# Optimization experiments

Measured on AMD Instinct MI355X. Metric: run time of the kernel, lower is better.

## Reference

```python
import jax, jax.numpy as jnp
import numpy as np

B_FACTOR = 4          # branching factor of the complete tree
DEPTH = 7             # levels 0..DEPTH; level DEPTH are leaves
N_NODES = (B_FACTOR ** (DEPTH + 1) - 1) // (B_FACTOR - 1)   # 21845
N_INTERNAL = (B_FACTOR ** DEPTH - 1) // (B_FACTOR - 1)      # 5461
IN_SIZE = 512
HID = 512
PARAM_SCALE = 0.02


def setup_inputs() -> dict:
    key = jax.random.key(0)
    ks = jax.random.split(key, 7)
    x = jax.random.normal(ks[0], (N_NODES, IN_SIZE), dtype=jnp.float32)
    # torch nn.Linear parameters: y = x @ W.T + b
    W_iou = jax.random.normal(ks[1], (3 * HID, IN_SIZE), dtype=jnp.float32) * PARAM_SCALE
    b_iou = jax.random.normal(ks[2], (3 * HID,), dtype=jnp.float32) * PARAM_SCALE
    W_f = jax.random.normal(ks[3], (HID, IN_SIZE), dtype=jnp.float32) * PARAM_SCALE
    b_f = jax.random.normal(ks[4], (HID,), dtype=jnp.float32) * PARAM_SCALE
    U_iou = jax.random.normal(ks[5], (3 * HID, HID), dtype=jnp.float32) * PARAM_SCALE
    U_f = jax.random.normal(ks[6], (HID, HID), dtype=jnp.float32) * PARAM_SCALE
    # children[j] = indices of the 4 children of internal node j (complete 4-ary tree)
    children = (B_FACTOR * jnp.arange(N_INTERNAL, dtype=jnp.int32)[:, None]
                + jnp.arange(1, B_FACTOR + 1, dtype=jnp.int32)[None, :])
    return {"x": x, "children": children, "W_iou": W_iou, "b_iou": b_iou,
            "W_f": W_f, "b_f": b_f, "U_iou": U_iou, "U_f": U_f}


def reference(x, children, W_iou, b_iou, W_f, b_f, U_iou, U_f):
    """Child-Sum Tree-LSTM over a complete 4-ary tree, processed level-batched
    bottom-up (equivalent to the per-node postorder recursion in the source).
    Leaves keep h = c = 0, as in the source (_forward_postorder returns early).
    NOTE: the source applies NO sigmoid to the forget gate term; we keep that.
    """
    N = x.shape[0]
    H = U_f.shape[0]
    # input-dependent parts are tree-independent: precompute once for all nodes
    wx_iou = x @ W_iou.T + b_iou          # [N, 3H]
    wx_f = x @ W_f.T + b_f                # [N, H]
    h = jnp.zeros((N, H), dtype=x.dtype)
    c = jnp.zeros_like(h)
    # level l occupies node indices [offs[l], offs[l+1]) — static constants
    offs = [(B_FACTOR ** l - 1) // (B_FACTOR - 1) for l in range(DEPTH + 2)]
    for l in range(DEPTH - 1, -1, -1):    # internal levels, deepest first
        s, e = offs[l], offs[l + 1]
        ch = children[s:e]                # [M, 4]
        h_ch = h[ch]                      # [M, 4, H] gather of child hidden states
        c_ch = c[ch]                      # [M, 4, H]
        h_sum = h_ch.sum(axis=1)          # child-sum
        iou = wx_iou[s:e] + h_sum @ U_iou.T               # [M, 3H]
        i, o, u = jnp.split(iou, 3, axis=-1)
        i = jax.nn.sigmoid(i)
        o = jax.nn.sigmoid(o)
        u = jnp.tanh(u)
        # forget term per child (no sigmoid, faithful to source)
        f = wx_f[s:e][:, None, :] + h_ch @ U_f.T          # [M, 4, H]
        c_new = i * u + (f * c_ch).sum(axis=1)            # [M, H]
        h = h.at[s:e].set(o * jnp.tanh(c_new))
        c = c.at[s:e].set(c_new)
    return h, c
```

## Files before the change

### kernel.cpp

```cpp
#include <hip/hip_runtime.h>
#include <cmath>

constexpr int N_NODES = 21845;
constexpr int N_INT   = 5461;
constexpr int HID     = 512;

typedef short  short8  __attribute__((ext_vector_type(8)));
typedef float  floatx4 __attribute__((ext_vector_type(4)));

__device__ __forceinline__ unsigned short f2bf(float f) {
    unsigned int u = __float_as_uint(f);
    u += 0x7fffu + ((u >> 16) & 1u);
    return (unsigned short)(u >> 16);
}

__global__ void prep_kernel(const float* __restrict__ x,
                            const float* __restrict__ W_iou,
                            const float* __restrict__ W_f,
                            const float* __restrict__ U_iou,
                            const float* __restrict__ U_f,
                            float* __restrict__ h_leaf,
                            float* __restrict__ c_leaf,
                            unsigned short* __restrict__ dstb)
{
    const size_t Z  = (size_t)(N_NODES - N_INT) * HID / 4;
    const size_t C0 = (size_t)N_INT * 512 / 4;
    const size_t C1 = C0 + 1536 * 512 / 4;
    const size_t C2 = C1 + 512 * 512 / 4;
    const size_t C3 = C2 + 1536 * 512 / 4;
    const size_t C4 = C3 + 512 * 512 / 4;
    const size_t total = 2 * Z + C4;
    size_t i = (size_t)blockIdx.x * blockDim.x + threadIdx.x;
    const size_t stride = (size_t)gridDim.x * blockDim.x;
    const float4 zz = {0.f, 0.f, 0.f, 0.f};
    for (; i < total; i += stride) {
        if (i < 2 * Z) {
            if (i < Z) ((float4*)h_leaf)[i] = zz;
            else       ((float4*)c_leaf)[i - Z] = zz;
        } else {
            size_t k = i - 2 * Z;
            const float* src; size_t off;
            if (k < C0)      { src = x;     off = k; }
            else if (k < C1) { src = W_iou; off = k - C0; }
            else if (k < C2) { src = W_f;   off = k - C1; }
            else if (k < C3) { src = U_iou; off = k - C2; }
            else             { src = U_f;   off = k - C3; }
            float4 v = ((const float4*)src)[off];
            ushort4 o;
            o.x = f2bf(v.x); o.y = f2bf(v.y); o.z = f2bf(v.z); o.w = f2bf(v.w);
            ((ushort4*)dstb)[k] = o;
        }
    }
}

#define GLD_LDS(g, l) __builtin_amdgcn_global_load_lds( \
    (const __attribute__((address_space(1))) void*)(g), \
    (__attribute__((address_space(3))) void*)(l), 16, 0, 0)

__device__ __forceinline__ void gemm_tile_128(
    const unsigned short* __restrict__ A, int Arows,
    const unsigned short* __restrict__ B,
    const float* __restrict__ bias,
    float* __restrict__ C, int ldc,
    int bm, int bn)
{
    __shared__ short8 AsV[1024];
    __shared__ short8 BsV[1024];

    const int tid  = threadIdx.x;
    const int wave = tid >> 6;
    const int lane = tid & 63;
    const int quad = lane >> 4;
    const int lr   = lane & 15;
    const int wr = (wave >> 1) * 64;
    const int wc = (wave & 1) * 64;

    floatx4 acc[4][4];
    #pragma unroll
    for (int i = 0; i < 4; ++i)
        #pragma unroll
        for (int j = 0; j < 4; ++j)
            acc[i][j] = (floatx4){0.f, 0.f, 0.f, 0.f};

    int s_row[4], s_gk[4];
    #pragma unroll
    for (int it = 0; it < 4; ++it) {
        int c = it * 256 + wave * 64 + lane;
        s_row[it] = c >> 3;
        s_gk[it]  = (c & 7) ^ (s_row[it] & 7);
    }

    for (int k0 = 0; k0 < 512; k0 += 64) {
        #pragma unroll
        for (int it = 0; it < 4; ++it) {
            int row = s_row[it];
            int gm = bm + row; if (gm >= Arows) gm = Arows - 1;
            GLD_LDS(A + (size_t)gm * 512 + k0 + s_gk[it] * 8, &AsV[it * 256 + wave * 64]);
            int gn = bn + row;
            GLD_LDS(B + (size_t)gn * 512 + k0 + s_gk[it] * 8, &BsV[it * 256 + wave * 64]);
        }
        __syncthreads();

        #pragma unroll
        for (int kc = 0; kc < 2; ++kc) {
            short8 af[4], bfr[4];
            const int q = kc * 4 + quad;
            #pragma unroll
            for (int mt = 0; mt < 4; ++mt) {
                int row = wr + mt * 16 + lr;
                af[mt] = AsV[row * 8 + (q ^ (row & 7))];
            }
            #pragma unroll
            for (int nt = 0; nt < 4; ++nt) {
                int row = wc + nt * 16 + lr;
                bfr[nt] = BsV[row * 8 + (q ^ (row & 7))];
            }
            #pragma unroll
            for (int mt = 0; mt < 4; ++mt)
                #pragma unroll
                for (int nt = 0; nt < 4; ++nt)
                    acc[mt][nt] = __builtin_amdgcn_mfma_f32_16x16x32_bf16(
                        af[mt], bfr[nt], acc[mt][nt], 0, 0, 0);
        }
        __syncthreads();
    }

    #pragma unroll
    for (int mt = 0; mt < 4; ++mt) {
        #pragma unroll
        for (int r = 0; r < 4; ++r) {
            int gm = bm + wr + mt * 16 + quad * 4 + r;
            if (gm >= Arows) continue;
            #pragma unroll
            for (int nt = 0; nt < 4; ++nt) {
                int gn = bn + wc + nt * 16 + lr;
                float v = acc[mt][nt][r];
                if (bias) v += bias[gn];
                C[(size_t)gm * ldc + gn] = v;
            }
        }
    }
}

__global__ __launch_bounds__(256) void wgemm_kernel(
    const unsigned short* __restrict__ xb,
    const unsigned short* __restrict__ Wib,
    const unsigned short* __restrict__ Wfb,
    const float* __restrict__ b_iou, const float* __restrict__ b_f,
    float* __restrict__ wx_iou, float* __restrict__ wx_f)
{
    int b = blockIdx.x;
    if (b < 516) {
        gemm_tile_128(xb, N_INT, Wib, b_iou, wx_iou, 1536, (b / 12) * 128, (b % 12) * 128);
    } else {
        int b2 = b - 516;
        gemm_tile_128(xb, 1365, Wfb, b_f, wx_f, 512, (b2 / 4) * 128, (b2 % 4) * 128);
    }
}

__global__ __launch_bounds__(256) void gemm5_kernel(
    const unsigned short* __restrict__ hs_bf,
    const unsigned short* __restrict__ h6_bf,
    const unsigned short* __restrict__ Uib, const unsigned short* __restrict__ Ufb,
    float* __restrict__ ioud, float* __restrict__ fd)
{
    int b = blockIdx.x;
    if (b < 96) {
        gemm_tile_128(hs_bf, 1024, Uib, nullptr, ioud, 1536, (b / 12) * 128, (b % 12) * 128);
    } else {
        int b2 = b - 96;
        gemm_tile_128(h6_bf, 4096, Ufb, nullptr, fd, 512, (b2 / 4) * 128, (b2 % 4) * 128);
    }
}

__global__ __launch_bounds__(256) void gemm4_kernel(
    const unsigned short* __restrict__ hs_bf,
    const unsigned short* __restrict__ h5_bf,
    const unsigned short* __restrict__ Uib, const unsigned short* __restrict__ Ufb,
    float* __restrict__ ioud, float* __restrict__ fd)
{
    int b = blockIdx.x;
    if (b < 24) {
        gemm_tile_128(hs_bf, 256, Uib, nullptr, ioud, 1536, (b / 12) * 128, (b % 12) * 128);
    } else {
        int b2 = b - 24;
        gemm_tile_128(h5_bf, 1024, Ufb, nullptr, fd, 512, (b2 / 4) * 128, (b2 % 4) * 128);
    }
}

__device__ __forceinline__ void direct_tile_16x64(
    const unsigned short* __restrict__ A, int Arows,
    const unsigned short* __restrict__ B,
    float* __restrict__ C, int ldc,
    int m0, int n0)
{
    const int lane = threadIdx.x & 63;
    const int quad = lane >> 4;
    const int lr   = lane & 15;
    int am = m0 + lr; if (am >= Arows) am = Arows - 1;
    const unsigned short* ap = A + (size_t)am * 512 + quad * 8;
    const unsigned short* bp = B + (size_t)(n0 + lr) * 512 + quad * 8;

    floatx4 acc[4];
    #pragma unroll
    for (int j = 0; j < 4; ++j) acc[j] = (floatx4){0.f, 0.f, 0.f, 0.f};

    #pragma unroll
    for (int k0 = 0; k0 < 512; k0 += 32) {
        short8 af = *(const short8*)(ap + k0);
        #pragma unroll
        for (int j = 0; j < 4; ++j) {
            short8 bf = *(const short8*)(bp + (size_t)j * 16 * 512 + k0);
            acc[j] = __builtin_amdgcn_mfma_f32_16x16x32_bf16(af, bf, acc[j], 0, 0, 0);
        }
    }

    #pragma unroll
    for (int j = 0; j < 4; ++j) {
        #pragma unroll
        for (int r = 0; r < 4; ++r) {
            int gm = m0 + quad * 4 + r;
            if (gm < Arows) C[(size_t)gm * ldc + n0 + j * 16 + lr] = acc[j][r];
        }
    }
}

__global__ __launch_bounds__(256) void gemm_small_kernel(
    const unsigned short* __restrict__ hs_bf,
    const unsigned short* __restrict__ hch_bf,
    const unsigned short* __restrict__ Uib, const unsigned short* __restrict__ Ufb,
    float* __restrict__ ioud, float* __restrict__ fd, int nl)
{
    const int w = blockIdx.x * 4 + (threadIdx.x >> 6);
    const int mI = (nl + 15) >> 4;
    const int nI = 1536 / 64;
    const int mF = (4 * nl + 15) >> 4;
    if (w < mI * nI) {
        direct_tile_16x64(hs_bf, nl, Uib, ioud, 1536, (w / nI) * 16, (w % nI) * 64);
    } else {
        int w2 = w - mI * nI;
        if (w2 < mF * 8)
            direct_tile_16x64(hch_bf, 4 * nl, Ufb, fd, 512, (w2 / 8) * 16, (w2 % 8) * 64);
    }
}

__global__ __launch_bounds__(512) void combine_wide_kernel(
    const float* __restrict__ wx_iou, const float* __restrict__ wx_f,
    const float* __restrict__ ioud, const float* __restrict__ fd,
    const float* __restrict__ c_child,
    float* __restrict__ h_out, float* __restrict__ c_out,
    unsigned short* __restrict__ h_bf, unsigned short* __restrict__ hs_bf,
    int s, int np)
{
    __shared__ float4 hsbuf[512];
    const int k  = threadIdx.x >> 7;
    const int jg = threadIdx.x & 127;
    const int j4 = jg << 2;
    const bool hasU = (ioud != nullptr);

    for (int tp = blockIdx.x; tp < np; tp += gridDim.x) {
        const int t = 4 * tp + k;
        const int n = s + t;
        const float* wrow = wx_iou + (size_t)n * 1536 + j4;
        float4 iv = *(const float4*)(wrow);
        float4 ov = *(const float4*)(wrow + 512);
        float4 uv = *(const float4*)(wrow + 1024);
        float4 fc = {0.f, 0.f, 0.f, 0.f};
        if (hasU) {
            const float* drow = ioud + (size_t)t * 1536 + j4;
            float4 a  = *(const float4*)(drow);
            float4 b  = *(const float4*)(drow + 512);
            float4 u2 = *(const float4*)(drow + 1024);
            float4 wf = *(const float4*)(wx_f + (size_t)n * 512 + j4);
            #pragma unroll
            for (int c = 0; c < 4; ++c) {
                ((float*)&iv)[c] += ((float*)&a)[c];
                ((float*)&ov)[c] += ((float*)&b)[c];
                ((float*)&uv)[c] += ((float*)&u2)[c];
            }
            #pragma unroll
            for (int q = 0; q < 4; ++q) {
                float4 f  = *(const float4*)(fd + (size_t)(4 * t + q) * 512 + j4);
                float4 cv = *(const float4*)(c_child + (size_t)(4 * t + q) * 512 + j4);
                #pragma unroll
                for (int c = 0; c < 4; ++c)
                    ((float*)&fc)[c] += (((float*)&wf)[c] + ((float*)&f)[c]) * ((float*)&cv)[c];
            }
        }
        float4 cn, hn; ushort4 hb;
        #pragma unroll
        for (int c = 0; c < 4; ++c) {
            float ig = 1.f / (1.f + expf(-((float*)&iv)[c]));
            float og = 1.f / (1.f + expf(-((float*)&ov)[c]));
            float ug = tanhf(((float*)&uv)[c]);
            float cv2 = ig * ug + ((float*)&fc)[c];
            float hv = og * tanhf(cv2);
            ((float*)&cn)[c] = cv2;
            ((float*)&hn)[c] = hv;
            ((unsigned short*)&hb)[c] = f2bf(hv);
        }
        *(float4*)(c_out + (size_t)n * 512 + j4) = cn;
        *(float4*)(h_out + (size_t)n * 512 + j4) = hn;
        *(ushort4*)(h_bf + (size_t)n * 512 + j4) = hb;
        hsbuf[threadIdx.x] = hn;
        __syncthreads();
        if (threadIdx.x < 128) {
            float4 s0 = hsbuf[jg], s1 = hsbuf[128 + jg], s2 = hsbuf[256 + jg], s3 = hsbuf[384 + jg];
            ushort4 ho;
            #pragma unroll
            for (int c = 0; c < 4; ++c)
                ((unsigned short*)&ho)[c] =
                    f2bf(((float*)&s0)[c] + ((float*)&s1)[c] + ((float*)&s2)[c] + ((float*)&s3)[c]);
            *(ushort4*)(hs_bf + (size_t)tp * 512 + j4) = ho;
        }
        __syncthreads();
    }
}

__global__ __launch_bounds__(128) void combine_root_kernel(
    const float* __restrict__ wx_iou, const float* __restrict__ wx_f,
    const float* __restrict__ ioud, const float* __restrict__ fd,
    const float* __restrict__ c_child,
    float* __restrict__ h_out, float* __restrict__ c_out)
{
    const int j4 = threadIdx.x << 2;
    float4 iv = *(const float4*)(wx_iou + j4);
    float4 ov = *(const float4*)(wx_iou + 512 + j4);
    float4 uv = *(const float4*)(wx_iou + 1024 + j4);
    float4 a  = *(const float4*)(ioud + j4);
    float4 b  = *(const float4*)(ioud + 512 + j4);
    float4 u2 = *(const float4*)(ioud + 1024 + j4);
    float4 wf = *(const float4*)(wx_f + j4);
    float4 fc = {0.f, 0.f, 0.f, 0.f};
    #pragma unroll
    for (int c = 0; c < 4; ++c) {
        ((float*)&iv)[c] += ((float*)&a)[c];
        ((float*)&ov)[c] += ((float*)&b)[c];
        ((float*)&uv)[c] += ((float*)&u2)[c];
    }
    #pragma unroll
    for (int q = 0; q < 4; ++q) {
        float4 f  = *(const float4*)(fd + (size_t)q * 512 + j4);
        float4 cv = *(const float4*)(c_child + (size_t)q * 512 + j4);
        #pragma unroll
        for (int c = 0; c < 4; ++c)
            ((float*)&fc)[c] += (((float*)&wf)[c] + ((float*)&f)[c]) * ((float*)&cv)[c];
    }
    float4 cn, hn;
    #pragma unroll
    for (int c = 0; c < 4; ++c) {
        float ig = 1.f / (1.f + expf(-((float*)&iv)[c]));
        float og = 1.f / (1.f + expf(-((float*)&ov)[c]));
        float ug = tanhf(((float*)&uv)[c]);
        float cv2 = ig * ug + ((float*)&fc)[c];
        ((float*)&cn)[c] = cv2;
        ((float*)&hn)[c] = og * tanhf(cv2);
    }
    *(float4*)(c_out + j4) = cn;
    *(float4*)(h_out + j4) = hn;
}

extern "C" void kernel_launch(void* const* d_in, const int* in_sizes, int n_in,
                              void* d_out, int out_size, void* d_ws, size_t ws_size,
                              hipStream_t stream) {
    const float* x     = (const float*)d_in[0];
    const float* W_iou = (const float*)d_in[2];
    const float* b_iou = (const float*)d_in[3];
    const float* W_f   = (const float*)d_in[4];
    const float* b_f   = (const float*)d_in[5];
    const float* U_iou = (const float*)d_in[6];
    const float* U_f   = (const float*)d_in[7];

    float* h_out = (float*)d_out;
    float* c_out = h_out + (size_t)N_NODES * HID;

    float* ws     = (float*)d_ws;
    float* wx_iou = ws;
    float* wx_f   = wx_iou + (size_t)N_INT * 1536;
    float* ioud   = wx_f   + (size_t)1365 * 512;
    float* fd     = ioud   + (size_t)1024 * 1536;
    unsigned short* xb   = (unsigned short*)(fd + (size_t)4096 * 512);
    unsigned short* Wib  = xb  + (size_t)N_INT * 512;
    unsigned short* Wfb  = Wib + (size_t)1536 * 512;
    unsigned short* Uib  = Wfb + (size_t)512 * 512;
    unsigned short* Ufb  = Uib + (size_t)1536 * 512;
    unsigned short* h_bf = Ufb + (size_t)512 * 512;
    unsigned short* hs_bf= h_bf + (size_t)N_INT * 512;

    const int offs[9] = {0, 1, 5, 21, 85, 341, 1365, 5461, 21845};

    prep_kernel<<<2048, 256, 0, stream>>>(x, W_iou, W_f, U_iou, U_f,
                                          h_out + (size_t)N_INT * HID,
                                          c_out + (size_t)N_INT * HID, xb);

    wgemm_kernel<<<516 + 44, 256, 0, stream>>>(xb, Wib, Wfb, b_iou, b_f, wx_iou, wx_f);

    combine_wide_kernel<<<1024, 512, 0, stream>>>(
        wx_iou, nullptr, nullptr, nullptr, nullptr,
        h_out, c_out, h_bf, hs_bf, 1365, 1024);

    gemm5_kernel<<<224, 256, 0, stream>>>(hs_bf, h_bf + (size_t)1365 * HID, Uib, Ufb, ioud, fd);
    combine_wide_kernel<<<256, 512, 0, stream>>>(
        wx_iou, wx_f, ioud, fd, c_out + (size_t)1365 * HID,
        h_out, c_out, h_bf, hs_bf, 341, 256);

    gemm4_kernel<<<56, 256, 0, stream>>>(hs_bf, h_bf + (size_t)341 * HID, Uib, Ufb, ioud, fd);
    combine_wide_kernel<<<64, 512, 0, stream>>>(
        wx_iou, wx_f, ioud, fd, c_out + (size_t)341 * HID,
        h_out, c_out, h_bf, hs_bf, 85, 64);

    for (int l = 3; l >= 1; --l) {
        const int s  = offs[l];
        const int nl = offs[l + 1] - s;
        const int cb = offs[l + 1];
        const int mI = (nl + 15) >> 4;
        const int mF = (4 * nl + 15) >> 4;
        const int waves = mI * 24 + mF * 8;
        gemm_small_kernel<<<(waves + 3) / 4, 256, 0, stream>>>(
            hs_bf, h_bf + (size_t)cb * HID, Uib, Ufb, ioud, fd, nl);
        combine_wide_kernel<<<(nl + 3) / 4, 512, 0, stream>>>(
            wx_iou, wx_f, ioud, fd, c_out + (size_t)cb * HID,
            h_out, c_out, h_bf, hs_bf, s, nl >> 2);
    }

    gemm_small_kernel<<<8, 256, 0, stream>>>(
        hs_bf, h_bf + (size_t)1 * HID, Uib, Ufb, ioud, fd, 1);
    combine_root_kernel<<<1, 128, 0, stream>>>(
        wx_iou, wx_f, ioud, fd, c_out + (size_t)1 * HID, h_out, c_out);
}
```

Baseline: 275.5 us.

## Fuse all tree levels into one persistent cooperative kernel with grid syncs

Replaces the sequence of about fifteen small kernel launches (prep, input GEMM, per-level recurrent GEMMs and combines, root) with one cooperative persistent kernel. Phases are separated by grid.sync, and grid-stride loops spread each phase's tiles over a grid sized from occupancy, capped at three blocks per CU. The goal is to remove launch gaps and tail idle time on the small upper levels. The cost is that the large input GEMM and prep now run under a capped grid with launch_bounds(256,2) register limits, and each grid-wide barrier carries its own overhead. A fallback multi-kernel path is kept, and the combine step is rewritten for 256 threads handling 8 columns each.

```diff
diff --git a/kernel.cpp b/kernel.cpp
--- a/kernel.cpp
+++ b/kernel.cpp
@@ -1,5 +1,8 @@
 #include <hip/hip_runtime.h>
+#include <hip/hip_cooperative_groups.h>
 #include <cmath>
+
+namespace cg = cooperative_groups;
 
 constexpr int N_NODES = 21845;
 constexpr int N_INT   = 5461;
@@ -14,14 +17,18 @@
     return (unsigned short)(u >> 16);
 }
 
-__global__ void prep_kernel(const float* __restrict__ x,
-                            const float* __restrict__ W_iou,
-                            const float* __restrict__ W_f,
-                            const float* __restrict__ U_iou,
-                            const float* __restrict__ U_f,
-                            float* __restrict__ h_leaf,
-                            float* __restrict__ c_leaf,
-                            unsigned short* __restrict__ dstb)
+#define GLD_LDS(g, l) __builtin_amdgcn_global_load_lds( \
+    (const __attribute__((address_space(1))) void*)(g), \
+    (__attribute__((address_space(3))) void*)(l), 16, 0, 0)
+
+__device__ __forceinline__ void prep_body(const float* __restrict__ x,
+                                          const float* __restrict__ W_iou,
+                                          const float* __restrict__ W_f,
+                                          const float* __restrict__ U_iou,
+                                          const float* __restrict__ U_f,
+                                          float* __restrict__ h_leaf,
+                                          float* __restrict__ c_leaf,
+                                          unsigned short* __restrict__ dstb)
 {
     const size_t Z  = (size_t)(N_NODES - N_INT) * HID / 4;
     const size_t C0 = (size_t)N_INT * 512 / 4;
@@ -53,10 +60,6 @@
     }
 }
 
-#define GLD_LDS(g, l) __builtin_amdgcn_global_load_lds( \
-    (const __attribute__((address_space(1))) void*)(g), \
-    (__attribute__((address_space(3))) void*)(l), 16, 0, 0)
-
 __device__ __forceinline__ void gemm_tile_128(
     const unsigned short* __restrict__ A, int Arows,
     const unsigned short* __restrict__ B,
@@ -142,6 +145,268 @@
     }
 }
 
+__device__ __forceinline__ void direct_tile_16x64(
+    const unsigned short* __restrict__ A, int Arows,
+    const unsigned short* __restrict__ B,
+    float* __restrict__ C, int ldc,
+    int m0, int n0)
+{
+    const int lane = threadIdx.x & 63;
+    const int quad = lane >> 4;
+    const int lr   = lane & 15;
+    int am = m0 + lr; if (am >= Arows) am = Arows - 1;
+    const unsigned short* ap = A + (size_t)am * 512 + quad * 8;
+    const unsigned short* bp = B + (size_t)(n0 + lr) * 512 + quad * 8;
+
+    floatx4 acc[4];
+    #pragma unroll
+    for (int j = 0; j < 4; ++j) acc[j] = (floatx4){0.f, 0.f, 0.f, 0.f};
+
+    #pragma unroll
+    for (int k0 = 0; k0 < 512; k0 += 32) {
+        short8 af = *(const short8*)(ap + k0);
+        #pragma unroll
+        for (int j = 0; j < 4; ++j) {
+            short8 bf = *(const short8*)(bp + (size_t)j * 16 * 512 + k0);
+            acc[j] = __builtin_amdgcn_mfma_f32_16x16x32_bf16(af, bf, acc[j], 0, 0, 0);
+        }
+    }
+
+    #pragma unroll
+    for (int j = 0; j < 4; ++j) {
+        #pragma unroll
+        for (int r = 0; r < 4; ++r) {
+            int gm = m0 + quad * 4 + r;
+            if (gm < Arows) C[(size_t)gm * ldc + n0 + j * 16 + lr] = acc[j][r];
+        }
+    }
+}
+
+__device__ __forceinline__ void small_gemm_phase(
+    const unsigned short* __restrict__ hs_bf,
+    const unsigned short* __restrict__ hch_bf,
+    const unsigned short* __restrict__ Uib, const unsigned short* __restrict__ Ufb,
+    float* __restrict__ ioud, float* __restrict__ fd, int nl)
+{
+    const int mI = (nl + 15) >> 4;
+    const int mF = (4 * nl + 15) >> 4;
+    const int totW = mI * 24 + mF * 8;
+    for (int w = blockIdx.x * 4 + (threadIdx.x >> 6); w < totW; w += gridDim.x * 4) {
+        if (w < mI * 24)
+            direct_tile_16x64(hs_bf, nl, Uib, ioud, 1536, (w / 24) * 16, (w % 24) * 64);
+        else {
+            int w2 = w - mI * 24;
+            direct_tile_16x64(hch_bf, 4 * nl, Ufb, fd, 512, (w2 / 8) * 16, (w2 % 8) * 64);
+        }
+    }
+}
+
+__device__ void combine_level_256(
+    const float* __restrict__ wx_iou, const float* __restrict__ wx_f,
+    const float* __restrict__ ioud, const float* __restrict__ fd,
+    const float* __restrict__ c_child,
+    float* __restrict__ h_out, float* __restrict__ c_out,
+    unsigned short* __restrict__ h_bf, unsigned short* __restrict__ hs_bf,
+    int s, int np, int hasU)
+{
+    __shared__ floatx4 hsbuf[512];
+    const int k  = threadIdx.x >> 6;
+    const int jg = threadIdx.x & 63;
+    const int j8 = jg << 3;
+
+    for (int tp = blockIdx.x; tp < np; tp += gridDim.x) {
+        const int t = 4 * tp + k;
+        const int n = s + t;
+        const float* wrow = wx_iou + (size_t)n * 1536 + j8;
+        floatx4 iv0 = *(const floatx4*)(wrow);
+        floatx4 iv1 = *(const floatx4*)(wrow + 4);
+        floatx4 ov0 = *(const floatx4*)(wrow + 512);
+        floatx4 ov1 = *(const floatx4*)(wrow + 516);
+        floatx4 uv0 = *(const floatx4*)(wrow + 1024);
+        floatx4 uv1 = *(const floatx4*)(wrow + 1028);
+        floatx4 fc0 = (floatx4){0.f,0.f,0.f,0.f};
+        floatx4 fc1 = (floatx4){0.f,0.f,0.f,0.f};
+        if (hasU) {
+            const float* drow = ioud + (size_t)t * 1536 + j8;
+            iv0 += *(const floatx4*)(drow);        iv1 += *(const floatx4*)(drow + 4);
+            ov0 += *(const floatx4*)(drow + 512);  ov1 += *(const floatx4*)(drow + 516);
+            uv0 += *(const floatx4*)(drow + 1024); uv1 += *(const floatx4*)(drow + 1028);
+            const float* wfp = wx_f + (size_t)n * 512 + j8;
+            floatx4 wf0 = *(const floatx4*)(wfp);
+            floatx4 wf1 = *(const floatx4*)(wfp + 4);
+            #pragma unroll
+            for (int q = 0; q < 4; ++q) {
+                const float* fp = fd + (size_t)(4 * t + q) * 512 + j8;
+                const float* cp = c_child + (size_t)(4 * t + q) * 512 + j8;
+                floatx4 f0 = *(const floatx4*)(fp),  f1 = *(const floatx4*)(fp + 4);
+                floatx4 cv0 = *(const floatx4*)(cp), cv1 = *(const floatx4*)(cp + 4);
+                fc0 += (wf0 + f0) * cv0;
+                fc1 += (wf1 + f1) * cv1;
+            }
+        }
+        floatx4 cn0, cn1, hn0, hn1;
+        #pragma unroll
+        for (int c = 0; c < 4; ++c) {
+            float ig = 1.f / (1.f + expf(-iv0[c]));
+            float og = 1.f / (1.f + expf(-ov0[c]));
+            float ug = tanhf(uv0[c]);
+            float cv2 = ig * ug + fc0[c];
+            cn0[c] = cv2;
+            hn0[c] = og * tanhf(cv2);
+        }
+        #pragma unroll
+        for (int c = 0; c < 4; ++c) {
+            float ig = 1.f / (1.f + expf(-iv1[c]));
+            float og = 1.f / (1.f + expf(-ov1[c]));
+            float ug = tanhf(uv1[c]);
+            float cv2 = ig * ug + fc1[c];
+            cn1[c] = cv2;
+            hn1[c] = og * tanhf(cv2);
+        }
+        float* cop = c_out + (size_t)n * 512 + j8;
+        float* hop = h_out + (size_t)n * 512 + j8;
+        *(floatx4*)(cop)     = cn0;  *(floatx4*)(cop + 4) = cn1;
+        *(floatx4*)(hop)     = hn0;  *(floatx4*)(hop + 4) = hn1;
+        ushort4 hb0, hb1;
+        hb0.x = f2bf(hn0[0]); hb0.y = f2bf(hn0[1]); hb0.z = f2bf(hn0[2]); hb0.w = f2bf(hn0[3]);
+        hb1.x = f2bf(hn1[0]); hb1.y = f2bf(hn1[1]); hb1.z = f2bf(hn1[2]); hb1.w = f2bf(hn1[3]);
+        *(ushort4*)(h_bf + (size_t)n * 512 + j8)     = hb0;
+        *(ushort4*)(h_bf + (size_t)n * 512 + j8 + 4) = hb1;
+
+        hsbuf[k * 128 + jg * 2]     = hn0;
+        hsbuf[k * 128 + jg * 2 + 1] = hn1;
+        __syncthreads();
+        if (threadIdx.x < 64) {
+            const int g = threadIdx.x;
+            floatx4 s0 = hsbuf[g*2]   + hsbuf[128 + g*2]   + hsbuf[256 + g*2]   + hsbuf[384 + g*2];
+            floatx4 s1 = hsbuf[g*2+1] + hsbuf[128 + g*2+1] + hsbuf[256 + g*2+1] + hsbuf[384 + g*2+1];
+            ushort4 o0, o1;
+            o0.x = f2bf(s0[0]); o0.y = f2bf(s0[1]); o0.z = f2bf(s0[2]); o0.w = f2bf(s0[3]);
+            o1.x = f2bf(s1[0]); o1.y = f2bf(s1[1]); o1.z = f2bf(s1[2]); o1.w = f2bf(s1[3]);
+            *(ushort4*)(hs_bf + (size_t)tp * 512 + g * 8)     = o0;
+            *(ushort4*)(hs_bf + (size_t)tp * 512 + g * 8 + 4) = o1;
+        }
+        __syncthreads();
+    }
+}
+
+__global__ __launch_bounds__(256, 2) void mega_kernel(
+    const float* __restrict__ x,
+    const float* __restrict__ W_iou, const float* __restrict__ b_iou,
+    const float* __restrict__ W_f,   const float* __restrict__ b_f,
+    const float* __restrict__ U_iou, const float* __restrict__ U_f,
+    float* __restrict__ h_out, float* __restrict__ c_out,
+    float* __restrict__ wx_iou, float* __restrict__ wx_f,
+    float* __restrict__ ioud, float* __restrict__ fd,
+    unsigned short* __restrict__ xb,
+    unsigned short* __restrict__ Wib, unsigned short* __restrict__ Wfb,
+    unsigned short* __restrict__ Uib, unsigned short* __restrict__ Ufb,
+    unsigned short* __restrict__ h_bf, unsigned short* __restrict__ hs_bf)
+{
+    cg::grid_group grid = cg::this_grid();
+
+    prep_body(x, W_iou, W_f, U_iou, U_f,
+              h_out + (size_t)N_INT * HID, c_out + (size_t)N_INT * HID, xb);
+    grid.sync();
+
+    for (int b = blockIdx.x; b < 560; b += gridDim.x) {
+        if (b < 516)
+            gemm_tile_128(xb, N_INT, Wib, b_iou, wx_iou, 1536, (b / 12) * 128, (b % 12) * 128);
+        else {
+            int b2 = b - 516;
+            gemm_tile_128(xb, 1365, Wfb, b_f, wx_f, 512, (b2 / 4) * 128, (b2 % 4) * 128);
+        }
+    }
+    grid.sync();
+
+    combine_level_256(wx_iou, nullptr, nullptr, nullptr, nullptr,
+                      h_out, c_out, h_bf, hs_bf, 1365, 1024, 0);
+    grid.sync();
+
+    for (int b = blockIdx.x; b < 224; b += gridDim.x) {
+        if (b < 96)
+            gemm_tile_128(hs_bf, 1024, Uib, nullptr, ioud, 1536, (b / 12) * 128, (b % 12) * 128);
+        else {
+            int b2 = b - 96;
+            gemm_tile_128(h_bf + (size_t)1365 * HID, 4096, Ufb, nullptr, fd, 512,
+                          (b2 / 4) * 128, (b2 % 4) * 128);
+        }
+    }
+    grid.sync();
+
+    combine_level_256(wx_iou, wx_f, ioud, fd, c_out + (size_t)1365 * HID,
+                      h_out, c_out, h_bf, hs_bf, 341, 256, 1);
+    grid.sync();
+
+    for (int b = blockIdx.x; b < 56; b += gridDim.x) {
+        if (b < 24)
+            gemm_tile_128(hs_bf, 256, Uib, nullptr, ioud, 1536, (b / 12) * 128, (b % 12) * 128);
+        else {
+            int b2 = b - 24;
+            gemm_tile_128(h_bf + (size_t)341 * HID, 1024, Ufb, nullptr, fd, 512,
+                          (b2 / 4) * 128, (b2 % 4) * 128);
+        }
+    }
+    grid.sync();
+
+    combine_level_256(wx_iou, wx_f, ioud, fd, c_out + (size_t)341 * HID,
+                      h_out, c_out, h_bf, hs_bf, 85, 64, 1);
+    grid.sync();
+
+    small_gemm_phase(hs_bf, h_bf + (size_t)85 * HID, Uib, Ufb, ioud, fd, 64);
+    grid.sync();
+    combine_level_256(wx_iou, wx_f, ioud, fd, c_out + (size_t)85 * HID,
+                      h_out, c_out, h_bf, hs_bf, 21, 16, 1);
+    grid.sync();
+    small_gemm_phase(hs_bf, h_bf + (size_t)21 * HID, Uib, Ufb, ioud, fd, 16);
+    grid.sync();
+    combine_level_256(wx_iou, wx_f, ioud, fd, c_out + (size_t)21 * HID,
+                      h_out, c_out, h_bf, hs_bf, 5, 4, 1);
+    grid.sync();
+    small_gemm_phase(hs_bf, h_bf + (size_t)5 * HID, Uib, Ufb, ioud, fd, 4);
+    grid.sync();
+    combine_level_256(wx_iou, wx_f, ioud, fd, c_out + (size_t)5 * HID,
+                      h_out, c_out, h_bf, hs_bf, 1, 1, 1);
+    grid.sync();
+
+    small_gemm_phase(hs_bf, h_bf + (size_t)1 * HID, Uib, Ufb, ioud, fd, 1);
+    grid.sync();
+
+    if (blockIdx.x == 0) {
+        const int j = threadIdx.x * 2;
+        #pragma unroll
+        for (int c = 0; c < 2; ++c) {
+            const int jj = j + c;
+            float iv = wx_iou[jj]        + ioud[jj];
+            float ov = wx_iou[512 + jj]  + ioud[512 + jj];
+            float uv = wx_iou[1024 + jj] + ioud[1024 + jj];
+            float wf = wx_f[jj];
+            float fc = 0.f;
+            #pragma unroll
+            for (int q = 0; q < 4; ++q)
+                fc += (wf + fd[(size_t)q * 512 + jj]) * c_out[(size_t)(q + 1) * 512 + jj];
+            float ig = 1.f / (1.f + expf(-iv));
+            float og = 1.f / (1.f + expf(-ov));
+            float ug = tanhf(uv);
+            float cv2 = ig * ug + fc;
+            c_out[jj] = cv2;
+            h_out[jj] = og * tanhf(cv2);
+        }
+    }
+}
+
+__global__ void prep_kernel(const float* __restrict__ x,
+                            const float* __restrict__ W_iou,
+                            const float* __restrict__ W_f,
+                            const float* __restrict__ U_iou,
+                            const float* __restrict__ U_f,
+                            float* __restrict__ h_leaf,
+                            float* __restrict__ c_leaf,
+                            unsigned short* __restrict__ dstb)
+{
+    prep_body(x, W_iou, W_f, U_iou, U_f, h_leaf, c_leaf, dstb);
+}
+
 __global__ __launch_bounds__(256) void wgemm_kernel(
     const unsigned short* __restrict__ xb,
     const unsigned short* __restrict__ Wib,
@@ -188,43 +453,6 @@
     }
 }
 
-__device__ __forceinline__ void direct_tile_16x64(
-    const unsigned short* __restrict__ A, int Arows,
-    const unsigned short* __restrict__ B,
-    float* __restrict__ C, int ldc,
-    int m0, int n0)
-{
-    const int lane = threadIdx.x & 63;
-    const int quad = lane >> 4;
-    const int lr   = lane & 15;
-    int am = m0 + lr; if (am >= Arows) am = Arows - 1;
-    const unsigned short* ap = A + (size_t)am * 512 + quad * 8;
-    const unsigned short* bp = B + (size_t)(n0 + lr) * 512 + quad * 8;
-
-    floatx4 acc[4];
-    #pragma unroll
-    for (int j = 0; j < 4; ++j) acc[j] = (floatx4){0.f, 0.f, 0.f, 0.f};
-
-    #pragma unroll
-    for (int k0 = 0; k0 < 512; k0 += 32) {
-        short8 af = *(const short8*)(ap + k0);
-        #pragma unroll
-        for (int j = 0; j < 4; ++j) {
-            short8 bf = *(const short8*)(bp + (size_t)j * 16 * 512 + k0);
-            acc[j] = __builtin_amdgcn_mfma_f32_16x16x32_bf16(af, bf, acc[j], 0, 0, 0);
-        }
-    }
-
-    #pragma unroll
-    for (int j = 0; j < 4; ++j) {
-        #pragma unroll
-        for (int r = 0; r < 4; ++r) {
-            int gm = m0 + quad * 4 + r;
-            if (gm < Arows) C[(size_t)gm * ldc + n0 + j * 16 + lr] = acc[j][r];
-        }
-    }
-}
-
 __global__ __launch_bounds__(256) void gemm_small_kernel(
     const unsigned short* __restrict__ hs_bf,
     const unsigned short* __restrict__ hch_bf,
@@ -233,88 +461,25 @@
 {
     const int w = blockIdx.x * 4 + (threadIdx.x >> 6);
     const int mI = (nl + 15) >> 4;
-    const int nI = 1536 / 64;
     const int mF = (4 * nl + 15) >> 4;
-    if (w < mI * nI) {
-        direct_tile_16x64(hs_bf, nl, Uib, ioud, 1536, (w / nI) * 16, (w % nI) * 64);
+    if (w < mI * 24) {
+        direct_tile_16x64(hs_bf, nl, Uib, ioud, 1536, (w / 24) * 16, (w % 24) * 64);
     } else {
-        int w2 = w - mI * nI;
+        int w2 = w - mI * 24;
         if (w2 < mF * 8)
             direct_tile_16x64(hch_bf, 4 * nl, Ufb, fd, 512, (w2 / 8) * 16, (w2 % 8) * 64);
     }
 }
 
-__global__ __launch_bounds__(512) void combine_wide_kernel(
+__global__ __launch_bounds__(256) void combine_kernel_fb(
     const float* __restrict__ wx_iou, const float* __restrict__ wx_f,
     const float* __restrict__ ioud, const float* __restrict__ fd,
     const float* __restrict__ c_child,
     float* __restrict__ h_out, float* __restrict__ c_out,
     unsigned short* __restrict__ h_bf, unsigned short* __restrict__ hs_bf,
-    int s, int np)
-{
-    __shared__ float4 hsbuf[512];
-    const int k  = threadIdx.x >> 7;
-    const int jg = threadIdx.x & 127;
-    const int j4 = jg << 2;
-    const bool hasU = (ioud != nullptr);
-
-    for (int tp = blockIdx.x; tp < np; tp += gridDim.x) {
-        const int t = 4 * tp + k;
-        const int n = s + t;
-        const float* wrow = wx_iou + (size_t)n * 1536 + j4;
-        float4 iv = *(const float4*)(wrow);
-        float4 ov = *(const float4*)(wrow + 512);
-        float4 uv = *(const float4*)(wrow + 1024);
-        float4 fc = {0.f, 0.f, 0.f, 0.f};
-        if (hasU) {
-            const float* drow = ioud + (size_t)t * 1536 + j4;
-            float4 a  = *(const float4*)(drow);
-            float4 b  = *(const float4*)(drow + 512);
-            float4 u2 = *(const float4*)(drow + 1024);
-            float4 wf = *(const float4*)(wx_f + (size_t)n * 512 + j4);
-            #pragma unroll
-            for (int c = 0; c < 4; ++c) {
-                ((float*)&iv)[c] += ((float*)&a)[c];
-                ((float*)&ov)[c] += ((float*)&b)[c];
-                ((float*)&uv)[c] += ((float*)&u2)[c];
-            }
-            #pragma unroll
-            for (int q = 0; q < 4; ++q) {
-                float4 f  = *(const float4*)(fd + (size_t)(4 * t + q) * 512 + j4);
-                float4 cv = *(const float4*)(c_child + (size_t)(4 * t + q) * 512 + j4);
-                #pragma unroll
-                for (int c = 0; c < 4; ++c)
-                    ((float*)&fc)[c] += (((float*)&wf)[c] + ((float*)&f)[c]) * ((float*)&cv)[c];
-            }
-        }
-        float4 cn, hn; ushort4 hb;
-        #pragma unroll
-        for (int c = 0; c < 4; ++c) {
-            float ig = 1.f / (1.f + expf(-((float*)&iv)[c]));
-            float og = 1.f / (1.f + expf(-((float*)&ov)[c]));
-            float ug = tanhf(((float*)&uv)[c]);
-            float cv2 = ig * ug + ((float*)&fc)[c];
-            float hv = og * tanhf(cv2);
-            ((float*)&cn)[c] = cv2;
-            ((float*)&hn)[c] = hv;
-            ((unsigned short*)&hb)[c] = f2bf(hv);
-        }
-        *(float4*)(c_out + (size_t)n * 512 + j4) = cn;
-        *(float4*)(h_out + (size_t)n * 512 + j4) = hn;
-        *(ushort4*)(h_bf + (size_t)n * 512 + j4) = hb;
-        hsbuf[threadIdx.x] = hn;
-        __syncthreads();
-        if (threadIdx.x < 128) {
-            float4 s0 = hsbuf[jg], s1 = hsbuf[128 + jg], s2 = hsbuf[256 + jg], s3 = hsbuf[384 + jg];
-            ushort4 ho;
-            #pragma unroll
-            for (int c = 0; c < 4; ++c)
-                ((unsigned short*)&ho)[c] =
-                    f2bf(((float*)&s0)[c] + ((float*)&s1)[c] + ((float*)&s2)[c] + ((float*)&s3)[c]);
-            *(ushort4*)(hs_bf + (size_t)tp * 512 + j4) = ho;
-        }
-        __syncthreads();
-    }
+    int s, int np, int hasU)
+{
+    combine_level_256(wx_iou, wx_f, ioud, fd, c_child, h_out, c_out, h_bf, hs_bf, s, np, hasU);
 }
 
 __global__ __launch_bounds__(128) void combine_root_kernel(
@@ -324,40 +489,24 @@
     float* __restrict__ h_out, float* __restrict__ c_out)
 {
     const int j4 = threadIdx.x << 2;
-    float4 iv = *(const float4*)(wx_iou + j4);
-    float4 ov = *(const float4*)(wx_iou + 512 + j4);
-    float4 uv = *(const float4*)(wx_iou + 1024 + j4);
-    float4 a  = *(const float4*)(ioud + j4);
-    float4 b  = *(const float4*)(ioud + 512 + j4);
-    float4 u2 = *(const float4*)(ioud + 1024 + j4);
-    float4 wf = *(const float4*)(wx_f + j4);
-    float4 fc = {0.f, 0.f, 0.f, 0.f};
     #pragma unroll
     for (int c = 0; c < 4; ++c) {
-        ((float*)&iv)[c] += ((float*)&a)[c];
-        ((float*)&ov)[c] += ((float*)&b)[c];
-        ((float*)&uv)[c] += ((float*)&u2)[c];
-    }
-    #pragma unroll
-    for (int q = 0; q < 4; ++q) {
-        float4 f  = *(const float4*)(fd + (size_t)q * 512 + j4);
-        float4 cv = *(const float4*)(c_child + (size_t)q * 512 + j4);
-        #pragma unroll
-        for (int c = 0; c < 4; ++c)
-            ((float*)&fc)[c] += (((float*)&wf)[c] + ((float*)&f)[c]) * ((float*)&cv)[c];
-    }
-    float4 cn, hn;
-    #pragma unroll
-    for (int c = 0; c < 4; ++c) {
-        float ig = 1.f / (1.f + expf(-((float*)&iv)[c]));
-        float og = 1.f / (1.f + expf(-((float*)&ov)[c]));
-        float ug = tanhf(((float*)&uv)[c]);
-        float cv2 = ig * ug + ((float*)&fc)[c];
-        ((float*)&cn)[c] = cv2;
-        ((float*)&hn)[c] = og * tanhf(cv2);
-    }
-    *(float4*)(c_out + j4) = cn;
-    *(float4*)(h_out + j4) = hn;
+        const int jj = j4 + c;
+        float iv = wx_iou[jj]        + ioud[jj];
+        float ov = wx_iou[512 + jj]  + ioud[512 + jj];
+        float uv = wx_iou[1024 + jj] + ioud[1024 + jj];
+        float wf = wx_f[jj];
+        float fc = 0.f;
+        #pragma unroll
+        for (int q = 0; q < 4; ++q)
+            fc += (wf + fd[(size_t)q * 512 + jj]) * c_child[(size_t)q * 512 + jj];
+        float ig = 1.f / (1.f + expf(-iv));
+        float og = 1.f / (1.f + expf(-ov));
+        float ug = tanhf(uv);
+        float cv2 = ig * ug + fc;
+        c_out[jj] = cv2;
+        h_out[jj] = og * tanhf(cv2);
+    }
 }
 
 extern "C" void kernel_launch(void* const* d_in, const int* in_sizes, int n_in,
@@ -387,44 +536,69 @@
     unsigned short* h_bf = Ufb + (size_t)512 * 512;
     unsigned short* hs_bf= h_bf + (size_t)N_INT * 512;
 
-    const int offs[9] = {0, 1, 5, 21, 85, 341, 1365, 5461, 21845};
-
-    prep_kernel<<<2048, 256, 0, stream>>>(x, W_iou, W_f, U_iou, U_f,
-                                          h_out + (size_t)N_INT * HID,
-                                          c_out + (size_t)N_INT * HID, xb);
-
-    wgemm_kernel<<<516 + 44, 256, 0, stream>>>(xb, Wib, Wfb, b_iou, b_f, wx_iou, wx_f);
-
-    combine_wide_kernel<<<1024, 512, 0, stream>>>(
-        wx_iou, nullptr, nullptr, nullptr, nullptr,
-        h_out, c_out, h_bf, hs_bf, 1365, 1024);
-
-    gemm5_kernel<<<224, 256, 0, stream>>>(hs_bf, h_bf + (size_t)1365 * HID, Uib, Ufb, ioud, fd);
-    combine_wide_kernel<<<256, 512, 0, stream>>>(
-        wx_iou, wx_f, ioud, fd, c_out + (size_t)1365 * HID,
-        h_out, c_out, h_bf, hs_bf, 341, 256);
-
-    gemm4_kernel<<<56, 256, 0, stream>>>(hs_bf, h_bf + (size_t)341 * HID, Uib, Ufb, ioud, fd);
-    combine_wide_kernel<<<64, 512, 0, stream>>>(
-        wx_iou, wx_f, ioud, fd, c_out + (size_t)341 * HID,
-        h_out, c_out, h_bf, hs_bf, 85, 64);
-
-    for (int l = 3; l >= 1; --l) {
-        const int s  = offs[l];
-        const int nl = offs[l + 1] - s;
-        const int cb = offs[l + 1];
-        const int mI = (nl + 15) >> 4;
-        const int mF = (4 * nl + 15) >> 4;
-        const int waves = mI * 24 + mF * 8;
-        gemm_small_kernel<<<(waves + 3) / 4, 256, 0, stream>>>(
-            hs_bf, h_bf + (size_t)cb * HID, Uib, Ufb, ioud, fd, nl);
-        combine_wide_kernel<<<(nl + 3) / 4, 512, 0, stream>>>(
-            wx_iou, wx_f, ioud, fd, c_out + (size_t)cb * HID,
-            h_out, c_out, h_bf, hs_bf, s, nl >> 2);
-    }
-
-    gemm_small_kernel<<<8, 256, 0, stream>>>(
-        hs_bf, h_bf + (size_t)1 * HID, Uib, Ufb, ioud, fd, 1);
-    combine_root_kernel<<<1, 128, 0, stream>>>(
-        wx_iou, wx_f, ioud, fd, c_out + (size_t)1 * HID, h_out, c_out);
-}
+    static int coopGrid = -1;
+    if (coopGrid == -1) {
+        int nb = 0;
+        hipError_t qe = hipOccupancyMaxActiveBlocksPerMultiprocessor(&nb, mega_kernel, 256, 0);
+        if (qe == hipSuccess && nb >= 1) {
+            if (nb > 3) nb = 3;
+            coopGrid = nb * 256;
+        } else {
+            coopGrid = 0;
+            (void)hipGetLastError();
+        }
+    }
+
+    bool launched = false;
+    if (coopGrid > 0) {
+        void* args[] = { (void*)&x, (void*)&W_iou, (void*)&b_iou, (void*)&W_f, (void*)&b_f,
+                         (void*)&U_iou, (void*)&U_f, (void*)&h_out, (void*)&c_out,
+                         (void*)&wx_iou, (void*)&wx_f, (void*)&ioud, (void*)&fd,
+                         (void*)&xb, (void*)&Wib, (void*)&Wfb, (void*)&Uib, (void*)&Ufb,
+                         (void*)&h_bf, (void*)&hs_bf };
+        hipError_t e = hipLaunchCooperativeKernel((const void*)mega_kernel,
+                                                  dim3(coopGrid), dim3(256), args, 0, stream);
+        if (e == hipSuccess) {
+            launched = true;
+        } else {
+            coopGrid = 0;
+            (void)hipGetLastError();
+        }
+    }
+
+    if (!launched) {
+        prep_kernel<<<2048, 256, 0, stream>>>(x, W_iou, W_f, U_iou, U_f,
+                                              h_out + (size_t)N_INT * HID,
+                                              c_out + (size_t)N_INT * HID, xb);
+        wgemm_kernel<<<516 + 44, 256, 0, stream>>>(xb, Wib, Wfb, b_iou, b_f, wx_iou, wx_f);
+        combine_kernel_fb<<<1024, 256, 0, stream>>>(
+            wx_iou, nullptr, nullptr, nullptr, nullptr,
+            h_out, c_out, h_bf, hs_bf, 1365, 1024, 0);
+        gemm5_kernel<<<224, 256, 0, stream>>>(hs_bf, h_bf + (size_t)1365 * HID, Uib, Ufb, ioud, fd);
+        combine_kernel_fb<<<256, 256, 0, stream>>>(
+            wx_iou, wx_f, ioud, fd, c_out + (size_t)1365 * HID,
+            h_out, c_out, h_bf, hs_bf, 341, 256, 1);
+        gemm4_kernel<<<56, 256, 0, stream>>>(hs_bf, h_bf + (size_t)341 * HID, Uib, Ufb, ioud, fd);
+        combine_kernel_fb<<<64, 256, 0, stream>>>(
+            wx_iou, wx_f, ioud, fd, c_out + (size_t)341 * HID,
+            h_out, c_out, h_bf, hs_bf, 85, 64, 1);
+        const int offs[9] = {0, 1, 5, 21, 85, 341, 1365, 5461, 21845};
+        for (int l = 3; l >= 1; --l) {
+            const int s  = offs[l];
+            const int nl = offs[l + 1] - s;
+            const int cb = offs[l + 1];
+            const int mI = (nl + 15) >> 4;
+            const int mF = (4 * nl + 15) >> 4;
+            const int waves = mI * 24 + mF * 8;
+            gemm_small_kernel<<<(waves + 3) / 4, 256, 0, stream>>>(
+                hs_bf, h_bf + (size_t)cb * HID, Uib, Ufb, ioud, fd, nl);
+            combine_kernel_fb<<<(nl + 3) / 4, 256, 0, stream>>>(
+                wx_iou, wx_f, ioud, fd, c_out + (size_t)cb * HID,
+                h_out, c_out, h_bf, hs_bf, s, nl >> 2, 1);
+        }
+        gemm_small_kernel<<<8, 256, 0, stream>>>(
+            hs_bf, h_bf + (size_t)1 * HID, Uib, Ufb, ioud, fd, 1);
+        combine_root_kernel<<<1, 128, 0, stream>>>(
+            wx_iou, wx_f, ioud, fd, c_out + (size_t)1 * HID, h_out, c_out);
+    }
+}
```

Result: slower. 704.4 us (+155.7%).
